# Kernel tuning notes

Measured on AMD Instinct MI355X. Metric: run time of the kernel, lower is better.

Reference implementation:

```python
import jax, jax.numpy as jnp
import numpy as np
import itertools

L, F, T = 16, 2, 2**19          # levels, features/level, hashmap size
BASE, SCALE = 16, 1.5           # base resolution, per-level scale
N = 524288                      # batch of sample points
PRIMES = np.array([1, 2654435761, 805459861, 3674653429], dtype=np.uint32)


def hash_encode(x, table):
    """Multi-resolution hash-grid encoding. x: [N,d] in [0,1); table: [L,T,F]."""
    n, d = x.shape
    corners = jnp.asarray(list(itertools.product([0, 1], repeat=d)), dtype=jnp.uint32)  # [C,d]
    primes = jnp.asarray(PRIMES[:d])
    is_hi = corners.astype(bool)[None]          # [1,C,d]
    outs = []
    for l in range(L):
        res = float(np.floor(BASE * SCALE**l))
        pos = x * res
        p0f = jnp.floor(pos)
        frac = pos - p0f                         # [N,d]
        p0 = p0f.astype(jnp.uint32)
        coords = p0[:, None, :] + corners[None]  # [N,C,d] uint32 (wraps)
        m = coords * primes                      # [N,C,d]
        h = m[..., 0]
        for j in range(1, d):
            h = h ^ m[..., j]
        idx = (h % np.uint32(T)).astype(jnp.int32)              # [N,C]
        w = jnp.where(is_hi, frac[:, None, :], 1.0 - frac[:, None, :]).prod(-1)  # [N,C]
        feat = table[l][idx]                                    # [N,C,F]
        outs.append(jnp.einsum('nc,ncf->nf', w, feat))
    return jnp.concatenate(outs, axis=-1)        # [N, L*F]


def mlp(h, w_in, w_hid, w_out):
    """tcnn-style bias-free MLP, ReLU hidden, linear output."""
    h = jax.nn.relu(h @ w_in)
    for i in range(w_hid.shape[0]):
        h = jax.nn.relu(h @ w_hid[i])
    return h @ w_out


def setup_inputs() -> dict:
    key = jax.random.key(0)
    ks = jax.random.split(key, 20)
    def w(k, shape):
        fan = shape[-2]
        return jax.random.normal(k, shape, jnp.float32) / np.sqrt(fan).astype(np.float32)
    return {
        'x': jax.random.uniform(ks[0], (N, 3), jnp.float32),
        't': jax.random.uniform(ks[1], (1,), jnp.float32),
        'skip_alpha': jax.random.uniform(ks[2], (1,), jnp.float32),
        'table_s': jax.random.normal(ks[3], (L, T, F), jnp.float32) * 1e-2,
        'ws_in': w(ks[4], (32, 64)),
        'ws_hid': w(ks[5], (3, 64, 64)),
        'ws_out': w(ks[6], (64, 64)),
        'table_d': jax.random.normal(ks[7], (L, T, F), jnp.float32) * 1e-2,
        'wd_in': w(ks[8], (32, 64)),
        'wd_hid': w(ks[9], (3, 64, 64)),
        'wd_out': w(ks[10], (64, 64)),
        'w1_in': w(ks[11], (128, 64)),
        'w1_hid': w(ks[12], (1, 64, 64)),
        'w1_out': w(ks[13], (64, 128)),
        'w2_in': w(ks[14], (128, 64)),
        'w2_hid': w(ks[15], (1, 64, 64)),
        'w2_out': w(ks[16], (64, 1)),
    }


def reference(x, t, skip_alpha, table_s, ws_in, ws_hid, ws_out,
              table_d, wd_in, wd_hid, wd_out,
              w1_in, w1_hid, w1_out, w2_in, w2_hid, w2_out):
    static_features = mlp(hash_encode(x, table_s), ws_in, ws_hid, ws_out)          # [N,64]
    t_col = jnp.broadcast_to(t, (x.shape[0], 1))
    x4 = jnp.concatenate([x, t_col], axis=1)                                        # [N,4]
    dynamic_features = mlp(hash_encode(x4, table_d), wd_in, wd_hid, wd_out)        # [N,64]
    features = jnp.concatenate([static_features, dynamic_features], axis=-1)       # [N,128]
    out1 = mlp(features, w1_in, w1_hid, w1_out)                                     # [N,128]
    blended = out1 * skip_alpha + (1.0 - skip_alpha) * features
    return mlp(blended, w2_in, w2_hid, w2_out)                                      # [N,1]
```

## Files before the change

### kernel.cpp

```cpp
#include <hip/hip_runtime.h>
#include <hip/hip_bf16.h>
#include <stdint.h>

#define LVLS 16
#define TSZ  524288
#define TMASK 0x7FFFFu
#define NPTS 524288
#define P1 2654435761u
#define P2 805459861u
#define P3 3674653429u

__constant__ float RES_TAB[16] = {
    16.f, 24.f, 36.f, 54.f, 81.f, 121.f, 182.f, 273.f,
    410.f, 615.f, 922.f, 1383.f, 2075.f, 3113.f, 4670.f, 7006.f};

using f16x8 = __attribute__((ext_vector_type(8))) _Float16;
using f32x4 = __attribute__((ext_vector_type(4))) float;

union PackF16 { uint32_t u; _Float16 h[2]; };

constexpr int PC = 136;

struct WPtrs { const float* p[11]; };

__global__ void k_weights(WPtrs wp, _Float16* __restrict__ dst) {
    int id = blockIdx.x * 256 + threadIdx.x;
    if (id >= 69632) return;
    const int OFF[16] = {0,2048,6144,10240,14336,18432,20480,24576,28672,
                         32768,36864,45056,49152,57344,65536,69632};
    const int KK[15]  = {32,64,64,64,64,32,64,64,64,64,128,64,64,128,64};
    const int NN[15]  = {64,64,64,64,64,64,64,64,64,64,64,64,128,64,64};
    const int PSEL[15]= {0,1,1,1,2,3,4,4,4,5,6,7,8,9,10};
    const int POFF[15]= {0,0,4096,8192,0,0,0,4096,8192,0,0,0,0,0,0};
    int m = 0;
    while (id >= OFF[m+1]) m++;
    int local = id - OFF[m];
    int j    = local & 7;
    int lane = (local >> 3) & 63;
    int blk  = local >> 9;
    int KC   = KK[m] >> 5;
    int ct   = blk / KC;
    int kc   = blk - ct * KC;
    int k    = kc*32 + ((lane>>4)<<3) + j;
    int n    = ct*16 + (lane & 15);
    const float* src = wp.p[PSEL[m]] + POFF[m];
    dst[id] = (_Float16)src[k * NN[m] + n];
}

__global__ void k_tables(const float* __restrict__ ts, const float* __restrict__ td,
                         const float* __restrict__ tptr, uint2* __restrict__ Tc) {
    int id = blockIdx.x * 256 + threadIdx.x;
    int l = id >> 19, i = id & TMASK;
    float2 sv = ((const float2*)ts)[id];
    float res = RES_TAB[l];
    float tv  = tptr[0];
    float pt  = tv * res;
    float fpt = floorf(pt);
    float ft  = pt - fpt;
    uint32_t ut = (uint32_t)(int)fpt;
    uint32_t h0 = (ut * P3) & TMASK;
    uint32_t h1 = ((ut + 1u) * P3) & TMASK;
    const float2* tdl = (const float2*)td + (size_t)l * TSZ;
    float2 a = tdl[i ^ h0];
    float2 b = tdl[i ^ h1];
    PackF16 o0, o1;
    o0.h[0] = (_Float16)sv.x; o0.h[1] = (_Float16)sv.y;
    o1.h[0] = (_Float16)((1.f - ft) * a.x + ft * b.x);
    o1.h[1] = (_Float16)((1.f - ft) * a.y + ft * b.y);
    Tc[id] = make_uint2(o0.u, o1.u);
}

__launch_bounds__(256)
__global__ void k_encode(const float* __restrict__ x,
                         const uint2* __restrict__ Tc,
                         uint32_t* __restrict__ EncS, uint32_t* __restrict__ EncD) {
    int tid  = threadIdx.x;
    int xcd  = blockIdx.x & 7;
    int slot = blockIdx.x >> 3;
    int gt   = slot * 256 + tid;
#pragma unroll
    for (int pass = 0; pass < 2; pass++) {
        int l = xcd * 2 + pass;
        float res = RES_TAB[l];
        const uint2* tcl = Tc + (size_t)l * TSZ;
        uint32_t* es = EncS + (size_t)l * NPTS;
        uint32_t* ed = EncD + (size_t)l * NPTS;
        for (int q = 0; q < 8; q++) {
            int p = gt + q * 65536;
            float px = x[p*3+0]*res, py = x[p*3+1]*res, pz = x[p*3+2]*res;
            float fx = floorf(px), fy = floorf(py), fz = floorf(pz);
            float wx = px-fx, wy = py-fy, wz = pz-fz;
            uint32_t ux = (uint32_t)(int)fx, uy = (uint32_t)(int)fy, uz = (uint32_t)(int)fz;
            uint32_t hx[2] = {ux, ux + 1u};
            uint32_t hy[2] = {uy * P1, (uy + 1u) * P1};
            uint32_t hz[2] = {uz * P2, (uz + 1u) * P2};
            uint2 v[8];
#pragma unroll
            for (int c = 0; c < 8; c++) {
                uint32_t idx = (hx[c&1] ^ hy[(c>>1)&1] ^ hz[c>>2]) & TMASK;
                v[c] = tcl[idx];
            }
            float wxa[2] = {1.f - wx, wx};
            float wya[2] = {1.f - wy, wy};
            float wza[2] = {1.f - wz, wz};
            float sA0 = 0.f, sA1 = 0.f, sD0 = 0.f, sD1 = 0.f;
#pragma unroll
            for (int c = 0; c < 8; c++) {
                float w = wxa[c&1] * wya[(c>>1)&1] * wza[c>>2];
                PackF16 s, d; s.u = v[c].x; d.u = v[c].y;
                sA0 += w * (float)s.h[0]; sA1 += w * (float)s.h[1];
                sD0 += w * (float)d.h[0]; sD1 += w * (float)d.h[1];
            }
            PackF16 o;
            o.h[0] = (_Float16)sA0; o.h[1] = (_Float16)sA1; es[p] = o.u;
            o.h[0] = (_Float16)sD0; o.h[1] = (_Float16)sD1; ed[p] = o.u;
        }
    }
}

__device__ __forceinline__ void wait_lds() {
    asm volatile("s_waitcnt lgkmcnt(0)" ::: "memory");
}

template<int KC, bool RELU>
__device__ __forceinline__ void mm_to_lds(const f16x8* a, const f16x8* __restrict__ W,
                                          _Float16* buf, int m, int quad, int lane) {
#pragma unroll
    for (int ct = 0; ct < 4; ct++) {
        f32x4 acc = {0.f, 0.f, 0.f, 0.f};
#pragma unroll
        for (int kc = 0; kc < KC; kc++)
            acc = __builtin_amdgcn_mfma_f32_16x16x32_f16(a[kc], W[(ct*KC+kc)*64+lane], acc, 0, 0, 0);
#pragma unroll
        for (int i = 0; i < 4; i++) {
            float v = acc[i];
            if (RELU) v = fmaxf(v, 0.f);
            buf[(quad*4+i)*PC + ct*16 + m] = (_Float16)v;
        }
    }
}

template<int KC>
__device__ __forceinline__ void mm_keep(const f16x8* a, const f16x8* __restrict__ W,
                                        _Float16* buf, PackF16* P, int m, int quad, int lane) {
#pragma unroll
    for (int ct = 0; ct < 4; ct++) {
        f32x4 acc = {0.f, 0.f, 0.f, 0.f};
#pragma unroll
        for (int kc = 0; kc < KC; kc++)
            acc = __builtin_amdgcn_mfma_f32_16x16x32_f16(a[kc], W[(ct*KC+kc)*64+lane], acc, 0, 0, 0);
#pragma unroll
        for (int ih = 0; ih < 2; ih++) {
            PackF16 pk;
            pk.h[0] = (_Float16)acc[ih*2+0];
            pk.h[1] = (_Float16)acc[ih*2+1];
            P[ct*2+ih] = pk;
            buf[(quad*4+ih*2+0)*PC + ct*16 + m] = pk.h[0];
            buf[(quad*4+ih*2+1)*PC + ct*16 + m] = pk.h[1];
        }
    }
}

template<int KC>
__device__ __forceinline__ void lds_to_afrag(const _Float16* buf, f16x8* a, int m, int quad) {
#pragma unroll
    for (int kc = 0; kc < KC; kc++)
        a[kc] = *(const f16x8*)(buf + m*PC + kc*32 + quad*8);
}

__device__ __forceinline__ void load_enc(const uint32_t* __restrict__ Enc,
                                         int pbase, int m, int quad, f16x8* a) {
    union { uint32_t u[4]; f16x8 v; } cv;
#pragma unroll
    for (int jj = 0; jj < 4; jj++)
        cv.u[jj] = Enc[(size_t)(quad*4+jj) * NPTS + pbase + m];
    a[0] = cv.v;
}

__launch_bounds__(256)
__global__ void k_mlp(const uint32_t* __restrict__ EncS, const uint32_t* __restrict__ EncD,
                      const _Float16* __restrict__ Wfrag, const float* __restrict__ alphap,
                      const float* __restrict__ w2out, float* __restrict__ out) {
    __shared__ _Float16 Sbuf[4][16*PC];
    __shared__ _Float16 Fbuf[4][16*PC];
    int tid  = threadIdx.x;
    int wave = tid >> 6, lane = tid & 63;
    int m = lane & 15, quad = lane >> 4;
    int pbase = blockIdx.x * 64 + wave * 16;
    _Float16* S = Sbuf[wave];
    _Float16* F = Fbuf[wave];
    const f16x8* W8 = (const f16x8*)Wfrag;

    f16x8 a[4];
    PackF16 sP[8], dP[8];

    load_enc(EncS, pbase, m, quad, a);
    mm_to_lds<1, true>(a, W8 + 0,    S, m, quad, lane); wait_lds();
    lds_to_afrag<2>(S, a, m, quad);
    mm_to_lds<2, true>(a, W8 + 256,  S, m, quad, lane); wait_lds();
    lds_to_afrag<2>(S, a, m, quad);
    mm_to_lds<2, true>(a, W8 + 768,  S, m, quad, lane); wait_lds();
    lds_to_afrag<2>(S, a, m, quad);
    mm_to_lds<2, true>(a, W8 + 1280, S, m, quad, lane); wait_lds();
    lds_to_afrag<2>(S, a, m, quad);
    mm_keep<2>(a, W8 + 1792, F, sP, m, quad, lane);
    load_enc(EncD, pbase, m, quad, a);
    mm_to_lds<1, true>(a, W8 + 2304, S, m, quad, lane); wait_lds();
    lds_to_afrag<2>(S, a, m, quad);
    mm_to_lds<2, true>(a, W8 + 2560, S, m, quad, lane); wait_lds();
    lds_to_afrag<2>(S, a, m, quad);
    mm_to_lds<2, true>(a, W8 + 3072, S, m, quad, lane); wait_lds();
    lds_to_afrag<2>(S, a, m, quad);
    mm_to_lds<2, true>(a, W8 + 3584, S, m, quad, lane); wait_lds();
    lds_to_afrag<2>(S, a, m, quad);
    mm_keep<2>(a, W8 + 4096, F + 64, dP, m, quad, lane);
    wait_lds();
    lds_to_afrag<4>(F, a, m, quad);
    mm_to_lds<4, true>(a, W8 + 4608, S, m, quad, lane); wait_lds();
    lds_to_afrag<2>(S, a, m, quad);
    mm_to_lds<2, true>(a, W8 + 5632, S, m, quad, lane); wait_lds();
    lds_to_afrag<2>(S, a, m, quad);
    float alpha = alphap[0];
#pragma unroll
    for (int ct = 0; ct < 8; ct++) {
        f32x4 acc = {0.f, 0.f, 0.f, 0.f};
#pragma unroll
        for (int kc = 0; kc < 2; kc++)
            acc = __builtin_amdgcn_mfma_f32_16x16x32_f16(a[kc], W8[6144 + (ct*2+kc)*64+lane], acc, 0, 0, 0);
#pragma unroll
        for (int i = 0; i < 4; i++) {
            float f = (ct < 4) ? (float)sP[ct*2 + (i>>1)].h[i&1]
                               : (float)dP[(ct-4)*2 + (i>>1)].h[i&1];
            F[(quad*4+i)*PC + ct*16 + m] = (_Float16)(alpha * acc[i] + (1.f - alpha) * f);
        }
    }
    wait_lds();
    lds_to_afrag<4>(F, a, m, quad);
    mm_to_lds<4, true>(a, W8 + 7168, S, m, quad, lane); wait_lds();
    lds_to_afrag<2>(S, a, m, quad);
    float rsum[4] = {0.f, 0.f, 0.f, 0.f};
#pragma unroll
    for (int ct = 0; ct < 4; ct++) {
        f32x4 acc = {0.f, 0.f, 0.f, 0.f};
#pragma unroll
        for (int kc = 0; kc < 2; kc++)
            acc = __builtin_amdgcn_mfma_f32_16x16x32_f16(a[kc], W8[8192 + (ct*2+kc)*64+lane], acc, 0, 0, 0);
        float wv = w2out[ct*16 + m];
#pragma unroll
        for (int i = 0; i < 4; i++)
            rsum[i] += fmaxf(acc[i], 0.f) * wv;
    }
#pragma unroll
    for (int off = 1; off < 16; off <<= 1) {
#pragma unroll
        for (int i = 0; i < 4; i++)
            rsum[i] += __shfl_xor(rsum[i], off, 64);
    }
    if (m == 0) {
#pragma unroll
        for (int i = 0; i < 4; i++)
            out[pbase + quad*4 + i] = rsum[i];
    }
}

extern "C" void kernel_launch(void* const* d_in, const int* in_sizes, int n_in,
                              void* d_out, int out_size, void* d_ws, size_t ws_size,
                              hipStream_t stream) {
    const float* x      = (const float*)d_in[0];
    const float* t      = (const float*)d_in[1];
    const float* alpha  = (const float*)d_in[2];
    const float* tab_s  = (const float*)d_in[3];
    const float* ws_in  = (const float*)d_in[4];
    const float* ws_hid = (const float*)d_in[5];
    const float* ws_out = (const float*)d_in[6];
    const float* tab_d  = (const float*)d_in[7];
    const float* wd_in  = (const float*)d_in[8];
    const float* wd_hid = (const float*)d_in[9];
    const float* wd_out = (const float*)d_in[10];
    const float* w1_in  = (const float*)d_in[11];
    const float* w1_hid = (const float*)d_in[12];
    const float* w1_out = (const float*)d_in[13];
    const float* w2_in  = (const float*)d_in[14];
    const float* w2_hid = (const float*)d_in[15];
    const float* w2_out = (const float*)d_in[16];
    float* out = (float*)d_out;

    char* ws = (char*)d_ws;
    _Float16* Wfrag = (_Float16*)ws;
    uint2*    Tc    = (uint2*)(ws + 139264);
    uint32_t* EncS  = (uint32_t*)(ws + 139264 + 67108864);
    uint32_t* EncD  = EncS + (size_t)LVLS * NPTS;
    size_t needed = 139264 + 67108864 + 2ull * 33554432ull;
    if (ws_size < needed) return;

    WPtrs wp;
    wp.p[0] = ws_in;  wp.p[1] = ws_hid; wp.p[2] = ws_out;
    wp.p[3] = wd_in;  wp.p[4] = wd_hid; wp.p[5] = wd_out;
    wp.p[6] = w1_in;  wp.p[7] = w1_hid; wp.p[8] = w1_out;
    wp.p[9] = w2_in;  wp.p[10] = w2_hid;

    k_weights<<<272,   256, 0, stream>>>(wp, Wfrag);
    k_tables <<<32768, 256, 0, stream>>>(tab_s, tab_d, t, Tc);
    k_encode <<<2048,  256, 0, stream>>>(x, Tc, EncS, EncD);
    k_mlp    <<<NPTS/64, 256, 0, stream>>>(EncS, EncD, Wfrag, alpha, w2_out, out);
}
```

Baseline: 639.1 us.

## Interleave static and dynamic MLP chains and batch two points per encode iteration

```diff
diff --git a/kernel.cpp b/kernel.cpp
--- a/kernel.cpp
+++ b/kernel.cpp
@@ -19,7 +19,8 @@
 
 union PackF16 { uint32_t u; _Float16 h[2]; };
 
-constexpr int PC = 136;
+constexpr int PS = 72;
+constexpr int PF = 136;
 
 struct WPtrs { const float* p[11]; };
 
@@ -76,8 +77,7 @@
                          uint32_t* __restrict__ EncS, uint32_t* __restrict__ EncD) {
     int tid  = threadIdx.x;
     int xcd  = blockIdx.x & 7;
-    int slot = blockIdx.x >> 3;
-    int gt   = slot * 256 + tid;
+    int gt   = (blockIdx.x >> 3) * 256 + tid;
 #pragma unroll
     for (int pass = 0; pass < 2; pass++) {
         int l = xcd * 2 + pass;
@@ -85,35 +85,50 @@
         const uint2* tcl = Tc + (size_t)l * TSZ;
         uint32_t* es = EncS + (size_t)l * NPTS;
         uint32_t* ed = EncD + (size_t)l * NPTS;
-        for (int q = 0; q < 8; q++) {
-            int p = gt + q * 65536;
-            float px = x[p*3+0]*res, py = x[p*3+1]*res, pz = x[p*3+2]*res;
-            float fx = floorf(px), fy = floorf(py), fz = floorf(pz);
-            float wx = px-fx, wy = py-fy, wz = pz-fz;
-            uint32_t ux = (uint32_t)(int)fx, uy = (uint32_t)(int)fy, uz = (uint32_t)(int)fz;
-            uint32_t hx[2] = {ux, ux + 1u};
-            uint32_t hy[2] = {uy * P1, (uy + 1u) * P1};
-            uint32_t hz[2] = {uz * P2, (uz + 1u) * P2};
-            uint2 v[8];
-#pragma unroll
-            for (int c = 0; c < 8; c++) {
-                uint32_t idx = (hx[c&1] ^ hy[(c>>1)&1] ^ hz[c>>2]) & TMASK;
-                v[c] = tcl[idx];
+        for (int q = 0; q < 4; q++) {
+            int p[2] = { gt + (2*q) * 65536, gt + (2*q+1) * 65536 };
+            uint32_t idx[2][8];
+            float wxa[2][2], wya[2][2], wza[2][2];
+#pragma unroll
+            for (int b = 0; b < 2; b++) {
+                float px = __builtin_nontemporal_load(x + p[b]*3 + 0) * res;
+                float py = __builtin_nontemporal_load(x + p[b]*3 + 1) * res;
+                float pz = __builtin_nontemporal_load(x + p[b]*3 + 2) * res;
+                float fx = floorf(px), fy = floorf(py), fz = floorf(pz);
+                float wx = px-fx, wy = py-fy, wz = pz-fz;
+                uint32_t ux = (uint32_t)(int)fx, uy = (uint32_t)(int)fy, uz = (uint32_t)(int)fz;
+                uint32_t hx[2] = {ux, ux + 1u};
+                uint32_t hy[2] = {uy * P1, (uy + 1u) * P1};
+                uint32_t hz[2] = {uz * P2, (uz + 1u) * P2};
+#pragma unroll
+                for (int c = 0; c < 8; c++)
+                    idx[b][c] = (hx[c&1] ^ hy[(c>>1)&1] ^ hz[c>>2]) & TMASK;
+                wxa[b][0] = 1.f-wx; wxa[b][1] = wx;
+                wya[b][0] = 1.f-wy; wya[b][1] = wy;
+                wza[b][0] = 1.f-wz; wza[b][1] = wz;
             }
-            float wxa[2] = {1.f - wx, wx};
-            float wya[2] = {1.f - wy, wy};
-            float wza[2] = {1.f - wz, wz};
-            float sA0 = 0.f, sA1 = 0.f, sD0 = 0.f, sD1 = 0.f;
-#pragma unroll
-            for (int c = 0; c < 8; c++) {
-                float w = wxa[c&1] * wya[(c>>1)&1] * wza[c>>2];
-                PackF16 s, d; s.u = v[c].x; d.u = v[c].y;
-                sA0 += w * (float)s.h[0]; sA1 += w * (float)s.h[1];
-                sD0 += w * (float)d.h[0]; sD1 += w * (float)d.h[1];
+            uint2 v[2][8];
+#pragma unroll
+            for (int b = 0; b < 2; b++)
+#pragma unroll
+                for (int c = 0; c < 8; c++)
+                    v[b][c] = tcl[idx[b][c]];
+#pragma unroll
+            for (int b = 0; b < 2; b++) {
+                float sA0 = 0.f, sA1 = 0.f, sD0 = 0.f, sD1 = 0.f;
+#pragma unroll
+                for (int c = 0; c < 8; c++) {
+                    float w = wxa[b][c&1] * wya[b][(c>>1)&1] * wza[b][c>>2];
+                    PackF16 s, d; s.u = v[b][c].x; d.u = v[b][c].y;
+                    sA0 += w * (float)s.h[0]; sA1 += w * (float)s.h[1];
+                    sD0 += w * (float)d.h[0]; sD1 += w * (float)d.h[1];
+                }
+                PackF16 o;
+                o.h[0] = (_Float16)sA0; o.h[1] = (_Float16)sA1;
+                __builtin_nontemporal_store(o.u, es + p[b]);
+                o.h[0] = (_Float16)sD0; o.h[1] = (_Float16)sD1;
+                __builtin_nontemporal_store(o.u, ed + p[b]);
             }
-            PackF16 o;
-            o.h[0] = (_Float16)sA0; o.h[1] = (_Float16)sA1; es[p] = o.u;
-            o.h[0] = (_Float16)sD0; o.h[1] = (_Float16)sD1; ed[p] = o.u;
         }
     }
 }
@@ -124,7 +139,7 @@
 
 template<int KC, bool RELU>
 __device__ __forceinline__ void mm_to_lds(const f16x8* a, const f16x8* __restrict__ W,
-                                          _Float16* buf, int m, int quad, int lane) {
+                                          _Float16* buf, int pitch, int m, int quad, int lane) {
 #pragma unroll
     for (int ct = 0; ct < 4; ct++) {
         f32x4 acc = {0.f, 0.f, 0.f, 0.f};
@@ -135,14 +150,15 @@
         for (int i = 0; i < 4; i++) {
             float v = acc[i];
             if (RELU) v = fmaxf(v, 0.f);
-            buf[(quad*4+i)*PC + ct*16 + m] = (_Float16)v;
+            buf[(quad*4+i)*pitch + ct*16 + m] = (_Float16)v;
         }
     }
 }
 
 template<int KC>
 __device__ __forceinline__ void mm_keep(const f16x8* a, const f16x8* __restrict__ W,
-                                        _Float16* buf, PackF16* P, int m, int quad, int lane) {
+                                        _Float16* buf, int pitch, PackF16* P,
+                                        int m, int quad, int lane) {
 #pragma unroll
     for (int ct = 0; ct < 4; ct++) {
         f32x4 acc = {0.f, 0.f, 0.f, 0.f};
@@ -155,17 +171,18 @@
             pk.h[0] = (_Float16)acc[ih*2+0];
             pk.h[1] = (_Float16)acc[ih*2+1];
             P[ct*2+ih] = pk;
-            buf[(quad*4+ih*2+0)*PC + ct*16 + m] = pk.h[0];
-            buf[(quad*4+ih*2+1)*PC + ct*16 + m] = pk.h[1];
+            buf[(quad*4+ih*2+0)*pitch + ct*16 + m] = pk.h[0];
+            buf[(quad*4+ih*2+1)*pitch + ct*16 + m] = pk.h[1];
         }
     }
 }
 
 template<int KC>
-__device__ __forceinline__ void lds_to_afrag(const _Float16* buf, f16x8* a, int m, int quad) {
+__device__ __forceinline__ void lds_to_afrag(const _Float16* buf, int pitch,
+                                             f16x8* a, int m, int quad) {
 #pragma unroll
     for (int kc = 0; kc < KC; kc++)
-        a[kc] = *(const f16x8*)(buf + m*PC + kc*32 + quad*8);
+        a[kc] = *(const f16x8*)(buf + m*pitch + kc*32 + quad*8);
 }
 
 __device__ __forceinline__ void load_enc(const uint32_t* __restrict__ Enc,
@@ -181,45 +198,47 @@
 __global__ void k_mlp(const uint32_t* __restrict__ EncS, const uint32_t* __restrict__ EncD,
                       const _Float16* __restrict__ Wfrag, const float* __restrict__ alphap,
                       const float* __restrict__ w2out, float* __restrict__ out) {
-    __shared__ _Float16 Sbuf[4][16*PC];
-    __shared__ _Float16 Fbuf[4][16*PC];
+    __shared__ _Float16 Sbuf[4][16*PS];
+    __shared__ _Float16 Fbuf[4][16*PF];
     int tid  = threadIdx.x;
     int wave = tid >> 6, lane = tid & 63;
     int m = lane & 15, quad = lane >> 4;
     int pbase = blockIdx.x * 64 + wave * 16;
     _Float16* S = Sbuf[wave];
     _Float16* F = Fbuf[wave];
+    _Float16* D = F + 64;
     const f16x8* W8 = (const f16x8*)Wfrag;
 
+    f16x8 aS[4], aD[4];
+    PackF16 sP[8], dP[8];
+
+    load_enc(EncS, pbase, m, quad, aS);
+    load_enc(EncD, pbase, m, quad, aD);
+    mm_to_lds<1, true>(aS, W8 + 0,    S, PS, m, quad, lane);
+    mm_to_lds<1, true>(aD, W8 + 2304, D, PF, m, quad, lane); wait_lds();
+    lds_to_afrag<2>(S, PS, aS, m, quad);
+    lds_to_afrag<2>(D, PF, aD, m, quad);
+    mm_to_lds<2, true>(aS, W8 + 256,  S, PS, m, quad, lane);
+    mm_to_lds<2, true>(aD, W8 + 2560, D, PF, m, quad, lane); wait_lds();
+    lds_to_afrag<2>(S, PS, aS, m, quad);
+    lds_to_afrag<2>(D, PF, aD, m, quad);
+    mm_to_lds<2, true>(aS, W8 + 768,  S, PS, m, quad, lane);
+    mm_to_lds<2, true>(aD, W8 + 3072, D, PF, m, quad, lane); wait_lds();
+    lds_to_afrag<2>(S, PS, aS, m, quad);
+    lds_to_afrag<2>(D, PF, aD, m, quad);
+    mm_to_lds<2, true>(aS, W8 + 1280, S, PS, m, quad, lane);
+    mm_to_lds<2, true>(aD, W8 + 3584, D, PF, m, quad, lane); wait_lds();
+    lds_to_afrag<2>(S, PS, aS, m, quad);
+    lds_to_afrag<2>(D, PF, aD, m, quad);
+    mm_keep<2>(aS, W8 + 1792, F, PF, sP, m, quad, lane);
+    mm_keep<2>(aD, W8 + 4096, D, PF, dP, m, quad, lane);
+    wait_lds();
     f16x8 a[4];
-    PackF16 sP[8], dP[8];
-
-    load_enc(EncS, pbase, m, quad, a);
-    mm_to_lds<1, true>(a, W8 + 0,    S, m, quad, lane); wait_lds();
-    lds_to_afrag<2>(S, a, m, quad);
-    mm_to_lds<2, true>(a, W8 + 256,  S, m, quad, lane); wait_lds();
-    lds_to_afrag<2>(S, a, m, quad);
-    mm_to_lds<2, true>(a, W8 + 768,  S, m, quad, lane); wait_lds();
-    lds_to_afrag<2>(S, a, m, quad);
-    mm_to_lds<2, true>(a, W8 + 1280, S, m, quad, lane); wait_lds();
-    lds_to_afrag<2>(S, a, m, quad);
-    mm_keep<2>(a, W8 + 1792, F, sP, m, quad, lane);
-    load_enc(EncD, pbase, m, quad, a);
-    mm_to_lds<1, true>(a, W8 + 2304, S, m, quad, lane); wait_lds();
-    lds_to_afrag<2>(S, a, m, quad);
-    mm_to_lds<2, true>(a, W8 + 2560, S, m, quad, lane); wait_lds();
-    lds_to_afrag<2>(S, a, m, quad);
-    mm_to_lds<2, true>(a, W8 + 3072, S, m, quad, lane); wait_lds();
-    lds_to_afrag<2>(S, a, m, quad);
-    mm_to_lds<2, true>(a, W8 + 3584, S, m, quad, lane); wait_lds();
-    lds_to_afrag<2>(S, a, m, quad);
-    mm_keep<2>(a, W8 + 4096, F + 64, dP, m, quad, lane);
-    wait_lds();
-    lds_to_afrag<4>(F, a, m, quad);
-    mm_to_lds<4, true>(a, W8 + 4608, S, m, quad, lane); wait_lds();
-    lds_to_afrag<2>(S, a, m, quad);
-    mm_to_lds<2, true>(a, W8 + 5632, S, m, quad, lane); wait_lds();
-    lds_to_afrag<2>(S, a, m, quad);
+    lds_to_afrag<4>(F, PF, a, m, quad);
+    mm_to_lds<4, true>(a, W8 + 4608, S, PS, m, quad, lane); wait_lds();
+    lds_to_afrag<2>(S, PS, a, m, quad);
+    mm_to_lds<2, true>(a, W8 + 5632, S, PS, m, quad, lane); wait_lds();
+    lds_to_afrag<2>(S, PS, a, m, quad);
     float alpha = alphap[0];
 #pragma unroll
     for (int ct = 0; ct < 8; ct++) {
@@ -231,13 +250,13 @@
         for (int i = 0; i < 4; i++) {
             float f = (ct < 4) ? (float)sP[ct*2 + (i>>1)].h[i&1]
                                : (float)dP[(ct-4)*2 + (i>>1)].h[i&1];
-            F[(quad*4+i)*PC + ct*16 + m] = (_Float16)(alpha * acc[i] + (1.f - alpha) * f);
+            F[(quad*4+i)*PF + ct*16 + m] = (_Float16)(alpha * acc[i] + (1.f - alpha) * f);
         }
     }
     wait_lds();
-    lds_to_afrag<4>(F, a, m, quad);
-    mm_to_lds<4, true>(a, W8 + 7168, S, m, quad, lane); wait_lds();
-    lds_to_afrag<2>(S, a, m, quad);
+    lds_to_afrag<4>(F, PF, a, m, quad);
+    mm_to_lds<4, true>(a, W8 + 7168, S, PS, m, quad, lane); wait_lds();
+    lds_to_afrag<2>(S, PS, a, m, quad);
     float rsum[4] = {0.f, 0.f, 0.f, 0.f};
 #pragma unroll
     for (int ct = 0; ct < 4; ct++) {
```

After: 652.9 us. +2.2%, slower.

## Restructure encode to point-major layout and stage MLP weights in LDS

Applied to the files above, without the earlier changes.

```diff
diff --git a/kernel.cpp b/kernel.cpp
--- a/kernel.cpp
+++ b/kernel.cpp
@@ -10,6 +10,9 @@
 #define P2 805459861u
 #define P3 3674653429u
 
+constexpr float RESC[16] = {
+    16.f, 24.f, 36.f, 54.f, 81.f, 121.f, 182.f, 273.f,
+    410.f, 615.f, 922.f, 1383.f, 2075.f, 3113.f, 4670.f, 7006.f};
 __constant__ float RES_TAB[16] = {
     16.f, 24.f, 36.f, 54.f, 81.f, 121.f, 182.f, 273.f,
     410.f, 615.f, 922.f, 1383.f, 2075.f, 3113.f, 4670.f, 7006.f};
@@ -19,7 +22,8 @@
 
 union PackF16 { uint32_t u; _Float16 h[2]; };
 
-constexpr int PC = 136;
+constexpr int PS = 72;
+constexpr int PF = 136;
 
 struct WPtrs { const float* p[11]; };
 
@@ -74,47 +78,45 @@
 __global__ void k_encode(const float* __restrict__ x,
                          const uint2* __restrict__ Tc,
                          uint32_t* __restrict__ EncS, uint32_t* __restrict__ EncD) {
-    int tid  = threadIdx.x;
-    int xcd  = blockIdx.x & 7;
-    int slot = blockIdx.x >> 3;
-    int gt   = slot * 256 + tid;
-#pragma unroll
-    for (int pass = 0; pass < 2; pass++) {
-        int l = xcd * 2 + pass;
-        float res = RES_TAB[l];
+    int p = blockIdx.x * 256 + threadIdx.x;
+    float x0 = x[p*3+0], x1 = x[p*3+1], x2 = x[p*3+2];
+    uint32_t outS[16], outD[16];
+#pragma unroll
+    for (int l = 0; l < LVLS; l++) {
+        const float res = RESC[l];
         const uint2* tcl = Tc + (size_t)l * TSZ;
-        uint32_t* es = EncS + (size_t)l * NPTS;
-        uint32_t* ed = EncD + (size_t)l * NPTS;
-        for (int q = 0; q < 8; q++) {
-            int p = gt + q * 65536;
-            float px = x[p*3+0]*res, py = x[p*3+1]*res, pz = x[p*3+2]*res;
-            float fx = floorf(px), fy = floorf(py), fz = floorf(pz);
-            float wx = px-fx, wy = py-fy, wz = pz-fz;
-            uint32_t ux = (uint32_t)(int)fx, uy = (uint32_t)(int)fy, uz = (uint32_t)(int)fz;
-            uint32_t hx[2] = {ux, ux + 1u};
-            uint32_t hy[2] = {uy * P1, (uy + 1u) * P1};
-            uint32_t hz[2] = {uz * P2, (uz + 1u) * P2};
-            uint2 v[8];
-#pragma unroll
-            for (int c = 0; c < 8; c++) {
-                uint32_t idx = (hx[c&1] ^ hy[(c>>1)&1] ^ hz[c>>2]) & TMASK;
-                v[c] = tcl[idx];
-            }
-            float wxa[2] = {1.f - wx, wx};
-            float wya[2] = {1.f - wy, wy};
-            float wza[2] = {1.f - wz, wz};
-            float sA0 = 0.f, sA1 = 0.f, sD0 = 0.f, sD1 = 0.f;
-#pragma unroll
-            for (int c = 0; c < 8; c++) {
-                float w = wxa[c&1] * wya[(c>>1)&1] * wza[c>>2];
-                PackF16 s, d; s.u = v[c].x; d.u = v[c].y;
-                sA0 += w * (float)s.h[0]; sA1 += w * (float)s.h[1];
-                sD0 += w * (float)d.h[0]; sD1 += w * (float)d.h[1];
-            }
-            PackF16 o;
-            o.h[0] = (_Float16)sA0; o.h[1] = (_Float16)sA1; es[p] = o.u;
-            o.h[0] = (_Float16)sD0; o.h[1] = (_Float16)sD1; ed[p] = o.u;
-        }
+        float px = x0*res, py = x1*res, pz = x2*res;
+        float fx = floorf(px), fy = floorf(py), fz = floorf(pz);
+        float wx = px-fx, wy = py-fy, wz = pz-fz;
+        uint32_t ux = (uint32_t)(int)fx, uy = (uint32_t)(int)fy, uz = (uint32_t)(int)fz;
+        uint32_t hx[2] = {ux, ux + 1u};
+        uint32_t hy[2] = {uy * P1, (uy + 1u) * P1};
+        uint32_t hz[2] = {uz * P2, (uz + 1u) * P2};
+        uint2 v[8];
+#pragma unroll
+        for (int c = 0; c < 8; c++) {
+            uint32_t idx = (hx[c&1] ^ hy[(c>>1)&1] ^ hz[c>>2]) & TMASK;
+            v[c] = tcl[idx];
+        }
+        float wxa[2] = {1.f-wx, wx}, wya[2] = {1.f-wy, wy}, wza[2] = {1.f-wz, wz};
+        float sA0 = 0.f, sA1 = 0.f, sD0 = 0.f, sD1 = 0.f;
+#pragma unroll
+        for (int c = 0; c < 8; c++) {
+            float w = wxa[c&1] * wya[(c>>1)&1] * wza[c>>2];
+            PackF16 s, d; s.u = v[c].x; d.u = v[c].y;
+            sA0 += w * (float)s.h[0]; sA1 += w * (float)s.h[1];
+            sD0 += w * (float)d.h[0]; sD1 += w * (float)d.h[1];
+        }
+        PackF16 o;
+        o.h[0] = (_Float16)sA0; o.h[1] = (_Float16)sA1; outS[l] = o.u;
+        o.h[0] = (_Float16)sD0; o.h[1] = (_Float16)sD1; outD[l] = o.u;
+    }
+    uint4* es = (uint4*)(EncS + (size_t)p * 16);
+    uint4* ed = (uint4*)(EncD + (size_t)p * 16);
+#pragma unroll
+    for (int i = 0; i < 4; i++) {
+        es[i] = make_uint4(outS[4*i], outS[4*i+1], outS[4*i+2], outS[4*i+3]);
+        ed[i] = make_uint4(outD[4*i], outD[4*i+1], outD[4*i+2], outD[4*i+3]);
     }
 }
 
@@ -123,144 +125,199 @@
 }
 
 template<int KC, bool RELU>
-__device__ __forceinline__ void mm_to_lds(const f16x8* a, const f16x8* __restrict__ W,
-                                          _Float16* buf, int m, int quad, int lane) {
+__device__ __forceinline__ void mm2(const f16x8 a[2][4], const f16x8* __restrict__ B,
+                                    _Float16* dst, int pitch,
+                                    int rbase, int m, int quad, int lane) {
 #pragma unroll
     for (int ct = 0; ct < 4; ct++) {
-        f32x4 acc = {0.f, 0.f, 0.f, 0.f};
+        f32x4 acc0 = {0.f,0.f,0.f,0.f}, acc1 = {0.f,0.f,0.f,0.f};
+#pragma unroll
+        for (int kc = 0; kc < KC; kc++) {
+            f16x8 b = B[(ct*KC+kc)*64 + lane];
+            acc0 = __builtin_amdgcn_mfma_f32_16x16x32_f16(a[0][kc], b, acc0, 0, 0, 0);
+            acc1 = __builtin_amdgcn_mfma_f32_16x16x32_f16(a[1][kc], b, acc1, 0, 0, 0);
+        }
+#pragma unroll
+        for (int i = 0; i < 4; i++) {
+            float v0 = acc0[i], v1 = acc1[i];
+            if (RELU) { v0 = fmaxf(v0, 0.f); v1 = fmaxf(v1, 0.f); }
+            dst[(rbase + 0*16 + quad*4+i)*pitch + ct*16 + m] = (_Float16)v0;
+            dst[(rbase + 1*16 + quad*4+i)*pitch + ct*16 + m] = (_Float16)v1;
+        }
+    }
+}
+
+template<int KC>
+__device__ __forceinline__ void mm2_keep(const f16x8 a[2][4], const f16x8* __restrict__ B,
+                                         _Float16* dst, int pitch, PackF16 P[2][8],
+                                         int rbase, int m, int quad, int lane) {
+#pragma unroll
+    for (int ct = 0; ct < 4; ct++) {
+        f32x4 acc0 = {0.f,0.f,0.f,0.f}, acc1 = {0.f,0.f,0.f,0.f};
+#pragma unroll
+        for (int kc = 0; kc < KC; kc++) {
+            f16x8 b = B[(ct*KC+kc)*64 + lane];
+            acc0 = __builtin_amdgcn_mfma_f32_16x16x32_f16(a[0][kc], b, acc0, 0, 0, 0);
+            acc1 = __builtin_amdgcn_mfma_f32_16x16x32_f16(a[1][kc], b, acc1, 0, 0, 0);
+        }
+#pragma unroll
+        for (int ih = 0; ih < 2; ih++) {
+            PackF16 p0, p1;
+            p0.h[0] = (_Float16)acc0[ih*2+0]; p0.h[1] = (_Float16)acc0[ih*2+1];
+            p1.h[0] = (_Float16)acc1[ih*2+0]; p1.h[1] = (_Float16)acc1[ih*2+1];
+            P[0][ct*2+ih] = p0; P[1][ct*2+ih] = p1;
+            dst[(rbase + 0*16 + quad*4+ih*2+0)*pitch + ct*16 + m] = p0.h[0];
+            dst[(rbase + 0*16 + quad*4+ih*2+1)*pitch + ct*16 + m] = p0.h[1];
+            dst[(rbase + 1*16 + quad*4+ih*2+0)*pitch + ct*16 + m] = p1.h[0];
+            dst[(rbase + 1*16 + quad*4+ih*2+1)*pitch + ct*16 + m] = p1.h[1];
+        }
+    }
+}
+
+template<int KC>
+__device__ __forceinline__ void read_a(const _Float16* buf, int pitch,
+                                       f16x8 a[2][4], int rbase, int m, int quad) {
+#pragma unroll
+    for (int rt = 0; rt < 2; rt++)
 #pragma unroll
         for (int kc = 0; kc < KC; kc++)
-            acc = __builtin_amdgcn_mfma_f32_16x16x32_f16(a[kc], W[(ct*KC+kc)*64+lane], acc, 0, 0, 0);
-#pragma unroll
-        for (int i = 0; i < 4; i++) {
-            float v = acc[i];
-            if (RELU) v = fmaxf(v, 0.f);
-            buf[(quad*4+i)*PC + ct*16 + m] = (_Float16)v;
-        }
-    }
-}
-
-template<int KC>
-__device__ __forceinline__ void mm_keep(const f16x8* a, const f16x8* __restrict__ W,
-                                        _Float16* buf, PackF16* P, int m, int quad, int lane) {
-#pragma unroll
-    for (int ct = 0; ct < 4; ct++) {
-        f32x4 acc = {0.f, 0.f, 0.f, 0.f};
-#pragma unroll
-        for (int kc = 0; kc < KC; kc++)
-            acc = __builtin_amdgcn_mfma_f32_16x16x32_f16(a[kc], W[(ct*KC+kc)*64+lane], acc, 0, 0, 0);
-#pragma unroll
-        for (int ih = 0; ih < 2; ih++) {
-            PackF16 pk;
-            pk.h[0] = (_Float16)acc[ih*2+0];
-            pk.h[1] = (_Float16)acc[ih*2+1];
-            P[ct*2+ih] = pk;
-            buf[(quad*4+ih*2+0)*PC + ct*16 + m] = pk.h[0];
-            buf[(quad*4+ih*2+1)*PC + ct*16 + m] = pk.h[1];
-        }
-    }
-}
-
-template<int KC>
-__device__ __forceinline__ void lds_to_afrag(const _Float16* buf, f16x8* a, int m, int quad) {
-#pragma unroll
-    for (int kc = 0; kc < KC; kc++)
-        a[kc] = *(const f16x8*)(buf + m*PC + kc*32 + quad*8);
-}
-
-__device__ __forceinline__ void load_enc(const uint32_t* __restrict__ Enc,
-                                         int pbase, int m, int quad, f16x8* a) {
-    union { uint32_t u[4]; f16x8 v; } cv;
-#pragma unroll
-    for (int jj = 0; jj < 4; jj++)
-        cv.u[jj] = Enc[(size_t)(quad*4+jj) * NPTS + pbase + m];
-    a[0] = cv.v;
-}
-
-__launch_bounds__(256)
+            a[rt][kc] = *(const f16x8*)(buf + (rbase + rt*16 + m)*pitch + kc*32 + quad*8);
+}
+
+__launch_bounds__(256, 4)
 __global__ void k_mlp(const uint32_t* __restrict__ EncS, const uint32_t* __restrict__ EncD,
                       const _Float16* __restrict__ Wfrag, const float* __restrict__ alphap,
                       const float* __restrict__ w2out, float* __restrict__ out) {
-    __shared__ _Float16 Sbuf[4][16*PC];
-    __shared__ _Float16 Fbuf[4][16*PC];
+    __shared__ f16x8    Wt[1024];
+    __shared__ _Float16 S [128*PS];
+    __shared__ _Float16 F [128*PF];
     int tid  = threadIdx.x;
     int wave = tid >> 6, lane = tid & 63;
     int m = lane & 15, quad = lane >> 4;
-    int pbase = blockIdx.x * 64 + wave * 16;
-    _Float16* S = Sbuf[wave];
-    _Float16* F = Fbuf[wave];
-    const f16x8* W8 = (const f16x8*)Wfrag;
-
-    f16x8 a[4];
-    PackF16 sP[8], dP[8];
-
-    load_enc(EncS, pbase, m, quad, a);
-    mm_to_lds<1, true>(a, W8 + 0,    S, m, quad, lane); wait_lds();
-    lds_to_afrag<2>(S, a, m, quad);
-    mm_to_lds<2, true>(a, W8 + 256,  S, m, quad, lane); wait_lds();
-    lds_to_afrag<2>(S, a, m, quad);
-    mm_to_lds<2, true>(a, W8 + 768,  S, m, quad, lane); wait_lds();
-    lds_to_afrag<2>(S, a, m, quad);
-    mm_to_lds<2, true>(a, W8 + 1280, S, m, quad, lane); wait_lds();
-    lds_to_afrag<2>(S, a, m, quad);
-    mm_keep<2>(a, W8 + 1792, F, sP, m, quad, lane);
-    load_enc(EncD, pbase, m, quad, a);
-    mm_to_lds<1, true>(a, W8 + 2304, S, m, quad, lane); wait_lds();
-    lds_to_afrag<2>(S, a, m, quad);
-    mm_to_lds<2, true>(a, W8 + 2560, S, m, quad, lane); wait_lds();
-    lds_to_afrag<2>(S, a, m, quad);
-    mm_to_lds<2, true>(a, W8 + 3072, S, m, quad, lane); wait_lds();
-    lds_to_afrag<2>(S, a, m, quad);
-    mm_to_lds<2, true>(a, W8 + 3584, S, m, quad, lane); wait_lds();
-    lds_to_afrag<2>(S, a, m, quad);
-    mm_keep<2>(a, W8 + 4096, F + 64, dP, m, quad, lane);
-    wait_lds();
-    lds_to_afrag<4>(F, a, m, quad);
-    mm_to_lds<4, true>(a, W8 + 4608, S, m, quad, lane); wait_lds();
-    lds_to_afrag<2>(S, a, m, quad);
-    mm_to_lds<2, true>(a, W8 + 5632, S, m, quad, lane); wait_lds();
-    lds_to_afrag<2>(S, a, m, quad);
+    int rbase = wave * 32;
+    int pbase = blockIdx.x * 128 + rbase;
+    const f16x8* Wg = (const f16x8*)Wfrag;
     float alpha = alphap[0];
+
+    f16x8 aS[2][4], aD[2][4];
+    PackF16 sP[2][8], dP[2][8];
+
+#pragma unroll
+    for (int rt = 0; rt < 2; rt++) {
+        aS[rt][0] = *(const f16x8*)(EncS + (size_t)(pbase + rt*16 + m)*16 + quad*4);
+        aD[rt][0] = *(const f16x8*)(EncD + (size_t)(pbase + rt*16 + m)*16 + quad*4);
+    }
+
+#define STAGE2(g0,c0,g1,c1)                                              \
+    __syncthreads();                                                     \
+    for (int i = tid; i < (c0); i += 256) Wt[i] = Wg[(g0)+i];            \
+    for (int i = tid; i < (c1); i += 256) Wt[(c0)+i] = Wg[(g1)+i];       \
+    __syncthreads();
+#define STAGE1(g0,c0)                                                    \
+    __syncthreads();                                                     \
+    for (int i = tid; i < (c0); i += 256) Wt[i] = Wg[(g0)+i];            \
+    __syncthreads();
+
+    _Float16* D = F + 64;
+
+    STAGE2(0, 256, 2304, 256)
+    mm2<1, true>(aS, Wt,       S, PS, rbase, m, quad, lane);
+    mm2<1, true>(aD, Wt + 256, D, PF, rbase, m, quad, lane);
+    wait_lds();
+    read_a<2>(S, PS, aS, rbase, m, quad);
+    read_a<2>(D, PF, aD, rbase, m, quad);
+    STAGE2(256, 512, 2560, 512)
+    mm2<2, true>(aS, Wt,       S, PS, rbase, m, quad, lane);
+    mm2<2, true>(aD, Wt + 512, D, PF, rbase, m, quad, lane);
+    wait_lds();
+    read_a<2>(S, PS, aS, rbase, m, quad);
+    read_a<2>(D, PF, aD, rbase, m, quad);
+    STAGE2(768, 512, 3072, 512)
+    mm2<2, true>(aS, Wt,       S, PS, rbase, m, quad, lane);
+    mm2<2, true>(aD, Wt + 512, D, PF, rbase, m, quad, lane);
+    wait_lds();
+    read_a<2>(S, PS, aS, rbase, m, quad);
+    read_a<2>(D, PF, aD, rbase, m, quad);
+    STAGE2(1280, 512, 3584, 512)
+    mm2<2, true>(aS, Wt,       S, PS, rbase, m, quad, lane);
+    mm2<2, true>(aD, Wt + 512, D, PF, rbase, m, quad, lane);
+    wait_lds();
+    read_a<2>(S, PS, aS, rbase, m, quad);
+    read_a<2>(D, PF, aD, rbase, m, quad);
+    STAGE2(1792, 512, 4096, 512)
+    mm2_keep<2>(aS, Wt,       F, PF, sP, rbase, m, quad, lane);
+    mm2_keep<2>(aD, Wt + 512, D, PF, dP, rbase, m, quad, lane);
+    wait_lds();
+    read_a<4>(F, PF, aS, rbase, m, quad);
+    STAGE1(4608, 1024)
+    mm2<4, true>(aS, Wt, S, PS, rbase, m, quad, lane);
+    wait_lds();
+    read_a<2>(S, PS, aS, rbase, m, quad);
+    STAGE1(5632, 512)
+    mm2<2, true>(aS, Wt, S, PS, rbase, m, quad, lane);
+    wait_lds();
+    read_a<2>(S, PS, aS, rbase, m, quad);
+    STAGE1(6144, 1024)
 #pragma unroll
     for (int ct = 0; ct < 8; ct++) {
-        f32x4 acc = {0.f, 0.f, 0.f, 0.f};
-#pragma unroll
-        for (int kc = 0; kc < 2; kc++)
-            acc = __builtin_amdgcn_mfma_f32_16x16x32_f16(a[kc], W8[6144 + (ct*2+kc)*64+lane], acc, 0, 0, 0);
-#pragma unroll
-        for (int i = 0; i < 4; i++) {
-            float f = (ct < 4) ? (float)sP[ct*2 + (i>>1)].h[i&1]
-                               : (float)dP[(ct-4)*2 + (i>>1)].h[i&1];
-            F[(quad*4+i)*PC + ct*16 + m] = (_Float16)(alpha * acc[i] + (1.f - alpha) * f);
-        }
-    }
-    wait_lds();
-    lds_to_afrag<4>(F, a, m, quad);
-    mm_to_lds<4, true>(a, W8 + 7168, S, m, quad, lane); wait_lds();
-    lds_to_afrag<2>(S, a, m, quad);
-    float rsum[4] = {0.f, 0.f, 0.f, 0.f};
+        f32x4 acc0 = {0.f,0.f,0.f,0.f}, acc1 = {0.f,0.f,0.f,0.f};
+#pragma unroll
+        for (int kc = 0; kc < 2; kc++) {
+            f16x8 b = Wt[(ct*2+kc)*64 + lane];
+            acc0 = __builtin_amdgcn_mfma_f32_16x16x32_f16(aS[0][kc], b, acc0, 0, 0, 0);
+            acc1 = __builtin_amdgcn_mfma_f32_16x16x32_f16(aS[1][kc], b, acc1, 0, 0, 0);
+        }
+#pragma unroll
+        for (int i = 0; i < 4; i++) {
+            float f0 = (ct < 4) ? (float)sP[0][ct*2 + (i>>1)].h[i&1]
+                                : (float)dP[0][(ct-4)*2 + (i>>1)].h[i&1];
+            float f1 = (ct < 4) ? (float)sP[1][ct*2 + (i>>1)].h[i&1]
+                                : (float)dP[1][(ct-4)*2 + (i>>1)].h[i&1];
+            F[(rbase + 0*16 + quad*4+i)*PF + ct*16 + m] = (_Float16)(alpha*acc0[i] + (1.f-alpha)*f0);
+            F[(rbase + 1*16 + quad*4+i)*PF + ct*16 + m] = (_Float16)(alpha*acc1[i] + (1.f-alpha)*f1);
+        }
+    }
+    wait_lds();
+    read_a<4>(F, PF, aS, rbase, m, quad);
+    STAGE1(7168, 1024)
+    mm2<4, true>(aS, Wt, S, PS, rbase, m, quad, lane);
+    wait_lds();
+    read_a<2>(S, PS, aS, rbase, m, quad);
+    STAGE1(8192, 512)
+    float rsum0[4] = {0.f,0.f,0.f,0.f}, rsum1[4] = {0.f,0.f,0.f,0.f};
 #pragma unroll
     for (int ct = 0; ct < 4; ct++) {
-        f32x4 acc = {0.f, 0.f, 0.f, 0.f};
-#pragma unroll
-        for (int kc = 0; kc < 2; kc++)
-            acc = __builtin_amdgcn_mfma_f32_16x16x32_f16(a[kc], W8[8192 + (ct*2+kc)*64+lane], acc, 0, 0, 0);
+        f32x4 acc0 = {0.f,0.f,0.f,0.f}, acc1 = {0.f,0.f,0.f,0.f};
+#pragma unroll
+        for (int kc = 0; kc < 2; kc++) {
+            f16x8 b = Wt[(ct*2+kc)*64 + lane];
+            acc0 = __builtin_amdgcn_mfma_f32_16x16x32_f16(aS[0][kc], b, acc0, 0, 0, 0);
+            acc1 = __builtin_amdgcn_mfma_f32_16x16x32_f16(aS[1][kc], b, acc1, 0, 0, 0);
+        }
         float wv = w2out[ct*16 + m];
 #pragma unroll
-        for (int i = 0; i < 4; i++)
-            rsum[i] += fmaxf(acc[i], 0.f) * wv;
+        for (int i = 0; i < 4; i++) {
+            rsum0[i] += fmaxf(acc0[i], 0.f) * wv;
+            rsum1[i] += fmaxf(acc1[i], 0.f) * wv;
+        }
     }
 #pragma unroll
     for (int off = 1; off < 16; off <<= 1) {
 #pragma unroll
-        for (int i = 0; i < 4; i++)
-            rsum[i] += __shfl_xor(rsum[i], off, 64);
+        for (int i = 0; i < 4; i++) {
+            rsum0[i] += __shfl_xor(rsum0[i], off, 64);
+            rsum1[i] += __shfl_xor(rsum1[i], off, 64);
+        }
     }
     if (m == 0) {
 #pragma unroll
-        for (int i = 0; i < 4; i++)
-            out[pbase + quad*4 + i] = rsum[i];
-    }
+        for (int i = 0; i < 4; i++) {
+            out[pbase + 0*16 + quad*4 + i] = rsum0[i];
+            out[pbase + 1*16 + quad*4 + i] = rsum1[i];
+        }
+    }
+#undef STAGE1
+#undef STAGE2
 }
 
 extern "C" void kernel_launch(void* const* d_in, const int* in_sizes, int n_in,
@@ -302,5 +359,5 @@
     k_weights<<<272,   256, 0, stream>>>(wp, Wfrag);
     k_tables <<<32768, 256, 0, stream>>>(tab_s, tab_d, t, Tc);
     k_encode <<<2048,  256, 0, stream>>>(x, Tc, EncS, EncD);
-    k_mlp    <<<NPTS/64, 256, 0, stream>>>(EncS, EncD, Wfrag, alpha, w2_out, out);
-}
+    k_mlp    <<<NPTS/128, 256, 0, stream>>>(EncS, EncD, Wfrag, alpha, w2_out, out);
+}
```

Result: slower. 739.8 us (+15.8%).
